# Kernel tuning notes

Measured on AMD Instinct MI355X. Metric: run time of the kernel, lower is better.

The kernel has to match this reference:

```python
import jax, jax.numpy as jnp
import numpy as np

EMB = 32
MP_ITERS = 5
N_NODES = 100000
N_EDGES = 3200000
N_FEAT = 128
N_ACT = 1024


def setup_inputs() -> dict:
    key = jax.random.key(0)
    ks = jax.random.split(key, 8)
    s = lambda fan_in: 1.0 / np.sqrt(fan_in)
    return {
        "node_feats": jax.random.normal(ks[0], (N_NODES, N_FEAT), dtype=jnp.float32),
        "edge_index": jax.random.randint(ks[1], (2, N_EDGES), 0, N_NODES, dtype=jnp.int64),
        "actionable": jax.random.randint(ks[2], (N_ACT,), 0, N_NODES, dtype=jnp.int64),
        "W_embed": jax.random.normal(ks[3], (N_FEAT, EMB), dtype=jnp.float32) * s(N_FEAT),
        "b_embed": jnp.zeros((EMB,), jnp.float32),
        "W_msg": jax.random.normal(ks[4], (EMB, EMB), dtype=jnp.float32) * s(EMB),
        "b_msg": jnp.zeros((EMB,), jnp.float32),
        "W_upd": jax.random.normal(ks[5], (2 * EMB, EMB), dtype=jnp.float32) * s(2 * EMB),
        "b_upd": jnp.zeros((EMB,), jnp.float32),
        "W_val": jax.random.normal(ks[6], (EMB, 1), dtype=jnp.float32) * s(EMB),
        "b_val": jnp.zeros((1,), jnp.float32),
        "W_pol": jax.random.normal(ks[7], (EMB, 1), dtype=jnp.float32) * s(EMB),
        "b_pol": jnp.zeros((1,), jnp.float32),
    }


def reference(node_feats, edge_index, actionable, W_embed, b_embed, W_msg, b_msg,
              W_upd, b_upd, W_val, b_val, W_pol, b_pol):
    lrelu = lambda z: jax.nn.leaky_relu(z, negative_slope=0.01)  # torch LeakyReLU default
    n = node_feats.shape[0]
    src, dst = edge_index[0], edge_index[1]
    # node embedding: (N, F) -> (N, 32)
    x = lrelu(node_feats @ W_embed + b_embed)
    # 5 message-passing iterations with shared weights:
    # m_{j->i} = MLP(x_j); agg_i = sum_j m_{j->i}; x_i' = U([x_i, agg_i])
    for _ in range(MP_ITERS):
        msgs = lrelu(x[src] @ W_msg + b_msg)               # (E, 32) gather + tiny GEMM
        agg = jax.ops.segment_sum(msgs, dst, num_segments=n)  # scatter-add -> (N, 32)
        x = lrelu(jnp.concatenate([x, agg], axis=1) @ W_upd + b_upd)
    xg = x.mean(axis=0, keepdims=True)                      # (1, 32)
    value = xg @ W_val + b_val                              # (1, 1)
    logits_all = (x @ W_pol + b_pol).ravel()                # (N,)
    probs = jax.nn.softmax(logits_all[actionable])          # (A,) action distribution
    # deterministic output: [value, action probabilities]
    return jnp.concatenate([value.ravel(), probs])
```

## Files before the change

### kernel.cpp

```cpp
#include <hip/hip_runtime.h>
#include <hip/hip_fp16.h>
#include <math.h>

#define EMB 32
#define NFEAT 128
#define RANGE 256
#define NBUCK_MAX 512
#define FILL_TILE 4096
#define FIN_CAP 12288
#define PAD_SLACK (RANGE * 10)

__device__ __forceinline__ float lrelu(float z) { return z > 0.f ? z : 0.01f * z; }

__global__ __launch_bounds__(256) void k_embed(
    const float* __restrict__ nf, const float* __restrict__ Wemb,
    const float* __restrict__ bemb, const float* __restrict__ Wmsg,
    const float* __restrict__ bmsg, float* __restrict__ x,
    __half* __restrict__ m, int n)
{
    __shared__ float sW[NFEAT * EMB];
    __shared__ float sWm[EMB * EMB];
    __shared__ float srow[8][NFEAT];
    int t = threadIdx.x;
    for (int i = t; i < NFEAT * EMB; i += 256) sW[i] = Wemb[i];
    for (int i = t; i < EMB * EMB; i += 256) sWm[i] = Wmsg[i];
    __syncthreads();

    int g = t >> 5;
    int e = t & 31;
    float be = bemb[e];
    float bm = bmsg[e];

    int per_pass = gridDim.x * 8;
    int iters = (n + per_pass - 1) / per_pass;
    for (int it = 0; it < iters; ++it) {
        int node = (it * gridDim.x + blockIdx.x) * 8 + g;
        __syncthreads();
        if (node < n) {
            float4 v = ((const float4*)(nf + (size_t)node * NFEAT))[e];
            ((float4*)&srow[g][0])[e] = v;
        }
        __syncthreads();
        if (node < n) {
            float acc = be;
            #pragma unroll
            for (int k = 0; k < NFEAT; ++k)
                acc = fmaf(srow[g][k], sW[k * EMB + e], acc);
            float xv = lrelu(acc);
            x[(size_t)node * EMB + e] = xv;
            float macc = bm;
            #pragma unroll
            for (int k = 0; k < EMB; ++k)
                macc = fmaf(__shfl(xv, k, 32), sWm[k * EMB + e], macc);
            m[(size_t)node * EMB + e] = __float2half(lrelu(macc));
        }
    }
}

__global__ __launch_bounds__(256) void k_bhist(
    const int* __restrict__ dst, int* __restrict__ bucket_cnt, int E, int nbuck)
{
    __shared__ int h[NBUCK_MAX];
    int t = threadIdx.x;
    for (int i = t; i < nbuck; i += 256) h[i] = 0;
    __syncthreads();
    for (int i = blockIdx.x * 256 + t; i < E; i += gridDim.x * 256)
        atomicAdd(&h[dst[i] >> 8], 1);
    __syncthreads();
    for (int i = t; i < nbuck; i += 256)
        if (h[i]) atomicAdd(&bucket_cnt[i], h[i]);
}

__global__ __launch_bounds__(512) void k_bscan(
    const int* __restrict__ bucket_cnt, int* __restrict__ bucket_base,
    int* __restrict__ bucket_cur, int nbuck)
{
    __shared__ int s[NBUCK_MAX];
    int t = threadIdx.x;
    int c = (t < nbuck) ? ((bucket_cnt[t] + PAD_SLACK + 16 + 15) & ~15) : 0;
    s[t] = c;
    __syncthreads();
    for (int off = 1; off < NBUCK_MAX; off <<= 1) {
        int add = (t >= off) ? s[t - off] : 0;
        __syncthreads();
        s[t] += add;
        __syncthreads();
    }
    if (t < nbuck) {
        int base = s[t] - c;
        bucket_base[t] = base;
        bucket_cur[t] = base;
    }
}

__global__ __launch_bounds__(256) void k_bfill(
    const int* __restrict__ src, const int* __restrict__ dst,
    int* __restrict__ bucket_cur, unsigned int* __restrict__ csrp, int E)
{
    __shared__ int scnt[NBUCK_MAX];
    __shared__ int gbase[NBUCK_MAX];
    int t = threadIdx.x;
    for (int i = t; i < NBUCK_MAX; i += 256) scnt[i] = 0;
    __syncthreads();

    unsigned int vals[16];
    int br[16];
    int base = blockIdx.x * FILL_TILE;
    #pragma unroll
    for (int k = 0; k < 16; ++k) {
        int e = base + k * 256 + t;
        if (e < E) {
            int d = dst[e];
            int s = src[e];
            int b = d >> 8;
            int r = atomicAdd(&scnt[b], 1);
            vals[k] = ((unsigned int)s << 8) | (unsigned int)(d & 255);
            br[k] = (b << 13) | r;
        } else br[k] = -1;
    }
    __syncthreads();
    for (int i = t; i < NBUCK_MAX; i += 256) {
        int c = scnt[i];
        gbase[i] = c ? atomicAdd(&bucket_cur[i], c) : 0;
    }
    __syncthreads();
    #pragma unroll
    for (int k = 0; k < 16; ++k) {
        if (br[k] >= 0) {
            int b = br[k] >> 13;
            int r = br[k] & 8191;
            csrp[gbase[b] + r] = vals[k];
        }
    }
}

__global__ __launch_bounds__(256) void k_csrfin(
    unsigned int* __restrict__ csrp, const int* __restrict__ bucket_base,
    const int* __restrict__ bucket_cnt, int* __restrict__ pdeg01,
    int* __restrict__ row, int n, int half)
{
    __shared__ int lh[2 * RANGE];
    __shared__ int pst[2 * RANGE];
    __shared__ int lc[2 * RANGE];
    __shared__ int psum[RANGE];
    __shared__ int ssrc[FIN_CAP];
    int bk = blockIdx.x;
    int t = threadIdx.x;
    int base = bucket_base[bk];
    int cnt = bucket_cnt[bk];
    if (cnt > FIN_CAP - PAD_SLACK) cnt = FIN_CAP - PAD_SLACK;

    lh[t] = 0;
    lh[t + RANGE] = 0;
    __syncthreads();
    for (int i = t; i < cnt; i += 256) {
        unsigned int v = csrp[base + i];
        int dl = (int)(v & 255u);
        int s = (int)(v >> 8);
        atomicAdd(&lh[dl * 2 + (s >= half ? 1 : 0)], 1);
    }
    __syncthreads();
    int c0 = lh[2 * t];
    int c1 = lh[2 * t + 1];
    int p0 = (c0 + 7) & ~7;
    int p1 = (c1 + 3) & ~3;
    psum[t] = p0 + p1;
    __syncthreads();
    for (int off = 1; off < RANGE; off <<= 1) {
        int add = (t >= off) ? psum[t - off] : 0;
        __syncthreads();
        psum[t] += add;
        __syncthreads();
    }
    int excl = psum[t] - (p0 + p1);
    pst[2 * t] = excl;
    pst[2 * t + 1] = excl + p0;
    lc[2 * t] = excl;
    lc[2 * t + 1] = excl + p0;
    int node = bk * RANGE + t;
    if (node < n) {
        row[node] = base + excl;
        pdeg01[node] = p0 | (p1 << 16);
    }
    __syncthreads();
    for (int i = t; i < cnt; i += 256) {
        unsigned int v = csrp[base + i];
        int dl = (int)(v & 255u);
        int s = (int)(v >> 8);
        int key = dl * 2 + (s >= half ? 1 : 0);
        int p = atomicAdd(&lc[key], 1);
        ssrc[p] = s;
    }
    __syncthreads();
    for (int i = c0; i < p0; ++i) ssrc[pst[2 * t] + i] = n;
    for (int i = c1; i < p1; ++i) ssrc[pst[2 * t + 1] + i] = n;
    __syncthreads();
    int ptot = psum[RANGE - 1];
    for (int i = t; i < ptot; i += 256)
        csrp[base + i] = (unsigned int)ssrc[i];
}

template<int PHASE>
__global__ __launch_bounds__(256) void k_gather(
    const __half* __restrict__ m_in, float* __restrict__ agg,
    const int* __restrict__ row, const int* __restrict__ pdeg01,
    const unsigned int* __restrict__ csrp, int n)
{
    int t = threadIdx.x;
    unsigned cp = (unsigned)(t & 15);
    int g = t >> 4;
    int groups = gridDim.x * 16;
    for (int node = blockIdx.x * 16 + g; node < n; node += groups) {
        int pd = pdeg01[node];
        int p0 = pd & 0xffff;
        float2 acc;
        if (PHASE == 0) {
            const uint4* ip = (const uint4*)(csrp + row[node]);
            int nch = p0 >> 3;
            acc.x = 0.f; acc.y = 0.f;
            for (int c = 0; c < nch; ++c) {
                uint4 ia = ip[2 * c];
                uint4 ib = ip[2 * c + 1];
                float2 f0 = __half22float2(*(const __half2*)(m_in + ia.x * 32u + 2u * cp));
                float2 f1 = __half22float2(*(const __half2*)(m_in + ia.y * 32u + 2u * cp));
                float2 f2 = __half22float2(*(const __half2*)(m_in + ia.z * 32u + 2u * cp));
                float2 f3 = __half22float2(*(const __half2*)(m_in + ia.w * 32u + 2u * cp));
                float2 f4 = __half22float2(*(const __half2*)(m_in + ib.x * 32u + 2u * cp));
                float2 f5 = __half22float2(*(const __half2*)(m_in + ib.y * 32u + 2u * cp));
                float2 f6 = __half22float2(*(const __half2*)(m_in + ib.z * 32u + 2u * cp));
                float2 f7 = __half22float2(*(const __half2*)(m_in + ib.w * 32u + 2u * cp));
                acc.x += ((f0.x + f1.x) + (f2.x + f3.x)) + ((f4.x + f5.x) + (f6.x + f7.x));
                acc.y += ((f0.y + f1.y) + (f2.y + f3.y)) + ((f4.y + f5.y) + (f6.y + f7.y));
            }
        } else {
            const uint4* ip = (const uint4*)(csrp + row[node] + p0);
            int nch = pd >> 18;
            acc = ((const float2*)agg)[(unsigned)node * 16u + cp];
            for (int c = 0; c < nch; ++c) {
                uint4 ia = ip[c];
                float2 f0 = __half22float2(*(const __half2*)(m_in + ia.x * 32u + 2u * cp));
                float2 f1 = __half22float2(*(const __half2*)(m_in + ia.y * 32u + 2u * cp));
                float2 f2 = __half22float2(*(const __half2*)(m_in + ia.z * 32u + 2u * cp));
                float2 f3 = __half22float2(*(const __half2*)(m_in + ia.w * 32u + 2u * cp));
                acc.x += (f0.x + f1.x) + (f2.x + f3.x);
                acc.y += (f0.y + f1.y) + (f2.y + f3.y);
            }
        }
        ((float2*)agg)[(unsigned)node * 16u + cp] = acc;
    }
}

__device__ __forceinline__ float2 gemm16(float2 v, const float* __restrict__ W, int cp)
{
    float2 u; u.x = 0.f; u.y = 0.f;
    #pragma unroll
    for (int kk = 0; kk < 16; ++kk) {
        float xa = __shfl(v.x, kk, 16);
        float xb = __shfl(v.y, kk, 16);
        float2 w0 = *(const float2*)&W[(2 * kk) * EMB + 2 * cp];
        float2 w1 = *(const float2*)&W[(2 * kk + 1) * EMB + 2 * cp];
        u.x = fmaf(xa, w0.x, u.x); u.y = fmaf(xa, w0.y, u.y);
        u.x = fmaf(xb, w1.x, u.x); u.y = fmaf(xb, w1.y, u.y);
    }
    return u;
}

template<int DO_MSG, int DO_COLSUM>
__global__ __launch_bounds__(256) void k_upd(
    float* __restrict__ x, const float* __restrict__ agg,
    __half* __restrict__ m_out,
    const float* __restrict__ Wupd, const float* __restrict__ bupd,
    const float* __restrict__ Wmsg, const float* __restrict__ bmsg,
    float* __restrict__ sums, int n)
{
    __shared__ float sW[2 * EMB * EMB];
    __shared__ float sWm[EMB * EMB];
    __shared__ float2 red[16][16];
    int t = threadIdx.x;
    for (int i = t; i < 2 * EMB * EMB; i += 256) sW[i] = Wupd[i];
    if (DO_MSG)
        for (int i = t; i < EMB * EMB; i += 256) sWm[i] = Wmsg[i];
    __syncthreads();

    int cp = t & 15;
    int g = t >> 4;
    float2 bu = ((const float2*)bupd)[cp];
    float2 bm2;
    if (DO_MSG) bm2 = ((const float2*)bmsg)[cp];
    float2 colacc; colacc.x = 0.f; colacc.y = 0.f;
    int groups = gridDim.x * 16;
    for (int node = blockIdx.x * 16 + g; node < n; node += groups) {
        float2 x2 = ((const float2*)x)[(unsigned)node * 16u + cp];
        float2 a2 = ((const float2*)agg)[(unsigned)node * 16u + cp];
        float2 u = gemm16(x2, sW, cp);
        float2 v = gemm16(a2, sW + EMB * EMB, cp);
        float2 xn;
        xn.x = lrelu(u.x + v.x + bu.x);
        xn.y = lrelu(u.y + v.y + bu.y);
        ((float2*)x)[(unsigned)node * 16u + cp] = xn;
        if (DO_MSG) {
            float2 mm = gemm16(xn, sWm, cp);
            mm.x = lrelu(mm.x + bm2.x);
            mm.y = lrelu(mm.y + bm2.y);
            *(__half2*)(m_out + (unsigned)node * 32u + 2u * cp) = __float22half2_rn(mm);
        }
        if (DO_COLSUM) { colacc.x += xn.x; colacc.y += xn.y; }
    }
    if (DO_COLSUM) {
        red[g][cp] = colacc;
        __syncthreads();
        if (t < 16) {
            float2 s2; s2.x = 0.f; s2.y = 0.f;
            #pragma unroll
            for (int gg = 0; gg < 16; ++gg) {
                s2.x += red[gg][t].x;
                s2.y += red[gg][t].y;
            }
            atomicAdd(&sums[2 * t], s2.x);
            atomicAdd(&sums[2 * t + 1], s2.y);
        }
    }
}

__global__ __launch_bounds__(1024) void k_head(
    const float* __restrict__ x, const int* __restrict__ act,
    const float* __restrict__ Wval, const float* __restrict__ bval,
    const float* __restrict__ Wpol, const float* __restrict__ bpol,
    const float* __restrict__ sums, float* __restrict__ out, int n, int A)
{
    __shared__ float sred[64];
    int t = threadIdx.x;
    int w = t >> 6;
    int lane = t & 63;
    int nwaves = (blockDim.x + 63) >> 6;

    float logit = -INFINITY;
    if (t < A) {
        int node = act[t];
        float acc = bpol[0];
        #pragma unroll
        for (int k = 0; k < EMB; ++k)
            acc = fmaf(x[(size_t)node * EMB + k], Wpol[k], acc);
        logit = acc;
    }
    float wm = logit;
    for (int off = 32; off; off >>= 1) wm = fmaxf(wm, __shfl_xor(wm, off, 64));
    if (lane == 0) sred[w] = wm;
    __syncthreads();
    if (t == 0) {
        float mm = -INFINITY;
        for (int i = 0; i < nwaves; ++i) mm = fmaxf(mm, sred[i]);
        sred[32] = mm;
    }
    __syncthreads();
    float bmax = sred[32];
    float ex = (t < A) ? __expf(logit - bmax) : 0.f;
    float ws = ex;
    for (int off = 32; off; off >>= 1) ws += __shfl_xor(ws, off, 64);
    if (lane == 0) sred[w] = ws;
    __syncthreads();
    if (t == 0) {
        float ss = 0.f;
        for (int i = 0; i < nwaves; ++i) ss += sred[i];
        sred[33] = ss;
        float val = bval[0];
        float inv_n = 1.f / (float)n;
        #pragma unroll
        for (int k = 0; k < EMB; ++k) val = fmaf(sums[k] * inv_n, Wval[k], val);
        out[0] = val;
    }
    __syncthreads();
    float tot = sred[33];
    if (t < A) out[1 + t] = ex / tot;
}

extern "C" void kernel_launch(void* const* d_in, const int* in_sizes, int n_in,
                              void* d_out, int out_size, void* d_ws, size_t ws_size,
                              hipStream_t stream)
{
    const float* nf   = (const float*)d_in[0];
    const int*   ei   = (const int*)d_in[1];
    const int*   act  = (const int*)d_in[2];
    const float* Wemb = (const float*)d_in[3];
    const float* bemb = (const float*)d_in[4];
    const float* Wmsg = (const float*)d_in[5];
    const float* bmsg = (const float*)d_in[6];
    const float* Wupd = (const float*)d_in[7];
    const float* bupd = (const float*)d_in[8];
    const float* Wval = (const float*)d_in[9];
    const float* bval = (const float*)d_in[10];
    const float* Wpol = (const float*)d_in[11];
    const float* bpol = (const float*)d_in[12];

    int n = in_sizes[0] / NFEAT;
    int E = in_sizes[1] / 2;
    int A = in_sizes[2];
    const int* src = ei;
    const int* dst = ei + E;
    int nbuck = (n + RANGE - 1) / RANGE;
    int half = n / 2;

    char* w = (char*)d_ws;
    auto alloc = [&](size_t bytes) -> void* {
        void* p = (void*)w;
        w += (bytes + 255) & ~(size_t)255;
        return p;
    };
    float*  x    = (float*)alloc((size_t)n * EMB * 4);
    float*  agg  = (float*)alloc((size_t)n * EMB * 4);
    __half* mA   = (__half*)alloc((size_t)(n + 1) * EMB * 2);
    __half* mB   = (__half*)alloc((size_t)(n + 1) * EMB * 2);
    int*    pdeg01 = (int*)alloc((size_t)n * 4);
    int*    row  = (int*)alloc((size_t)n * 4);
    int*    bucket_cnt  = (int*)alloc((size_t)nbuck * 4);
    int*    bucket_base = (int*)alloc((size_t)nbuck * 4);
    int*    bucket_cur  = (int*)alloc((size_t)nbuck * 4);
    unsigned int* csrp  = (unsigned int*)alloc(((size_t)E + (size_t)nbuck * (PAD_SLACK + 32)) * 4);
    float*  sums = (float*)alloc(EMB * 4);

    hipMemsetAsync(bucket_cnt, 0, (size_t)nbuck * 4, stream);
    hipMemsetAsync(sums, 0, EMB * 4, stream);
    hipMemsetAsync(mA + (size_t)n * EMB, 0, EMB * 2, stream);
    hipMemsetAsync(mB + (size_t)n * EMB, 0, EMB * 2, stream);

    const int NB = 2048;

    k_embed<<<NB, 256, 0, stream>>>(nf, Wemb, bemb, Wmsg, bmsg, x, mA, n);

    k_bhist<<<256, 256, 0, stream>>>(dst, bucket_cnt, E, nbuck);
    k_bscan<<<1, NBUCK_MAX, 0, stream>>>(bucket_cnt, bucket_base, bucket_cur, nbuck);
    int nfill = (E + FILL_TILE - 1) / FILL_TILE;
    k_bfill<<<nfill, 256, 0, stream>>>(src, dst, bucket_cur, csrp, E);
    k_csrfin<<<nbuck, 256, 0, stream>>>(csrp, bucket_base, bucket_cnt, pdeg01, row, n, half);

    __half* mi = mA;
    __half* mo = mB;
    for (int it = 0; it < 5; ++it) {
        k_gather<0><<<NB, 256, 0, stream>>>(mi, agg, row, pdeg01, csrp, n);
        k_gather<1><<<NB, 256, 0, stream>>>(mi, agg, row, pdeg01, csrp, n);
        if (it < 4)
            k_upd<1, 0><<<NB, 256, 0, stream>>>(x, agg, mo, Wupd, bupd, Wmsg, bmsg, sums, n);
        else
            k_upd<0, 1><<<NB, 256, 0, stream>>>(x, agg, mo, Wupd, bupd, Wmsg, bmsg, sums, n);
        __half* tmp = mi; mi = mo; mo = tmp;
    }

    k_head<<<1, 1024, 0, stream>>>(x, act, Wval, bval, Wpol, bpol, sums,
                                   (float*)d_out, n, A);
}
```

Baseline: 682.0 us.

## Widen per-thread vectors to 8-byte half loads in gather and embed kernels

```diff
diff --git a/kernel.cpp b/kernel.cpp
--- a/kernel.cpp
+++ b/kernel.cpp
@@ -8,7 +8,7 @@
 #define NBUCK_MAX 512
 #define FILL_TILE 4096
 #define FIN_CAP 12288
-#define PAD_SLACK (RANGE * 10)
+#define PAD_SLACK (RANGE * 14)
 
 __device__ __forceinline__ float lrelu(float z) { return z > 0.f ? z : 0.01f * z; }
 
@@ -20,40 +20,60 @@
 {
     __shared__ float sW[NFEAT * EMB];
     __shared__ float sWm[EMB * EMB];
-    __shared__ float srow[8][NFEAT];
     int t = threadIdx.x;
     for (int i = t; i < NFEAT * EMB; i += 256) sW[i] = Wemb[i];
     for (int i = t; i < EMB * EMB; i += 256) sWm[i] = Wmsg[i];
     __syncthreads();
 
-    int g = t >> 5;
-    int e = t & 31;
-    float be = bemb[e];
-    float bm = bmsg[e];
-
-    int per_pass = gridDim.x * 8;
-    int iters = (n + per_pass - 1) / per_pass;
-    for (int it = 0; it < iters; ++it) {
-        int node = (it * gridDim.x + blockIdx.x) * 8 + g;
-        __syncthreads();
-        if (node < n) {
-            float4 v = ((const float4*)(nf + (size_t)node * NFEAT))[e];
-            ((float4*)&srow[g][0])[e] = v;
-        }
-        __syncthreads();
-        if (node < n) {
-            float acc = be;
-            #pragma unroll
-            for (int k = 0; k < NFEAT; ++k)
-                acc = fmaf(srow[g][k], sW[k * EMB + e], acc);
-            float xv = lrelu(acc);
-            x[(size_t)node * EMB + e] = xv;
-            float macc = bm;
-            #pragma unroll
-            for (int k = 0; k < EMB; ++k)
-                macc = fmaf(__shfl(xv, k, 32), sWm[k * EMB + e], macc);
-            m[(size_t)node * EMB + e] = __float2half(lrelu(macc));
-        }
+    int c = t & 7;
+    int g = t >> 3;
+    float4 be = ((const float4*)bemb)[c];
+    float4 bm = ((const float4*)bmsg)[c];
+
+    int per_pass = gridDim.x * 32;
+    for (int node = blockIdx.x * 32 + g; node < n; node += per_pass) {
+        float v[16];
+        const float4* rp = (const float4*)(nf + (size_t)node * NFEAT + c * 16);
+        #pragma unroll
+        for (int q = 0; q < 4; ++q) {
+            float4 r4 = rp[q];
+            v[4 * q + 0] = r4.x; v[4 * q + 1] = r4.y;
+            v[4 * q + 2] = r4.z; v[4 * q + 3] = r4.w;
+        }
+        float4 acc = be;
+        #pragma unroll
+        for (int k = 0; k < NFEAT; ++k) {
+            float xa = __shfl(v[k & 15], k >> 4, 8);
+            float4 wv = *(const float4*)&sW[k * EMB + 4 * c];
+            acc.x = fmaf(xa, wv.x, acc.x);
+            acc.y = fmaf(xa, wv.y, acc.y);
+            acc.z = fmaf(xa, wv.z, acc.z);
+            acc.w = fmaf(xa, wv.w, acc.w);
+        }
+        float xn[4];
+        xn[0] = lrelu(acc.x); xn[1] = lrelu(acc.y);
+        xn[2] = lrelu(acc.z); xn[3] = lrelu(acc.w);
+        float4 xs; xs.x = xn[0]; xs.y = xn[1]; xs.z = xn[2]; xs.w = xn[3];
+        ((float4*)x)[(unsigned)node * 8u + (unsigned)c] = xs;
+
+        float4 ma = bm;
+        #pragma unroll
+        for (int k = 0; k < EMB; ++k) {
+            float xa = __shfl(xn[k & 3], k >> 2, 8);
+            float4 wv = *(const float4*)&sWm[k * EMB + 4 * c];
+            ma.x = fmaf(xa, wv.x, ma.x);
+            ma.y = fmaf(xa, wv.y, ma.y);
+            ma.z = fmaf(xa, wv.z, ma.z);
+            ma.w = fmaf(xa, wv.w, ma.w);
+        }
+        float2 m0; m0.x = lrelu(ma.x); m0.y = lrelu(ma.y);
+        float2 m1; m1.x = lrelu(ma.z); m1.y = lrelu(ma.w);
+        __half2 h0 = __float22half2_rn(m0);
+        __half2 h1 = __float22half2_rn(m1);
+        uint2 st;
+        st.x = *(unsigned*)&h0;
+        st.y = *(unsigned*)&h1;
+        *(uint2*)(m + (unsigned)node * 32u + 4u * (unsigned)c) = st;
     }
 }
 
@@ -163,7 +183,7 @@
     int c0 = lh[2 * t];
     int c1 = lh[2 * t + 1];
     int p0 = (c0 + 7) & ~7;
-    int p1 = (c1 + 3) & ~3;
+    int p1 = (c1 + 7) & ~7;
     psum[t] = p0 + p1;
     __syncthreads();
     for (int off = 1; off < RANGE; off <<= 1) {
@@ -200,6 +220,17 @@
         csrp[base + i] = (unsigned int)ssrc[i];
 }
 
+__device__ __forceinline__ void gacc(const __half* __restrict__ mp,
+                                     unsigned idx, unsigned c4, float4& acc)
+{
+    uint2 r = *(const uint2*)(mp + idx * 32u + c4);
+    __half2 h0 = *(__half2*)&r.x;
+    __half2 h1 = *(__half2*)&r.y;
+    float2 f0 = __half22float2(h0);
+    float2 f1 = __half22float2(h1);
+    acc.x += f0.x; acc.y += f0.y; acc.z += f1.x; acc.w += f1.y;
+}
+
 template<int PHASE>
 __global__ __launch_bounds__(256) void k_gather(
     const __half* __restrict__ m_in, float* __restrict__ agg,
@@ -207,46 +238,37 @@
     const unsigned int* __restrict__ csrp, int n)
 {
     int t = threadIdx.x;
-    unsigned cp = (unsigned)(t & 15);
-    int g = t >> 4;
-    int groups = gridDim.x * 16;
-    for (int node = blockIdx.x * 16 + g; node < n; node += groups) {
+    unsigned c4 = (unsigned)((t & 7) * 4);
+    int g = t >> 3;
+    int groups = gridDim.x * 32;
+    for (int node = blockIdx.x * 32 + g; node < n; node += groups) {
         int pd = pdeg01[node];
         int p0 = pd & 0xffff;
-        float2 acc;
+        const uint4* ip;
+        int nch;
+        float4 acc;
         if (PHASE == 0) {
-            const uint4* ip = (const uint4*)(csrp + row[node]);
-            int nch = p0 >> 3;
-            acc.x = 0.f; acc.y = 0.f;
-            for (int c = 0; c < nch; ++c) {
-                uint4 ia = ip[2 * c];
-                uint4 ib = ip[2 * c + 1];
-                float2 f0 = __half22float2(*(const __half2*)(m_in + ia.x * 32u + 2u * cp));
-                float2 f1 = __half22float2(*(const __half2*)(m_in + ia.y * 32u + 2u * cp));
-                float2 f2 = __half22float2(*(const __half2*)(m_in + ia.z * 32u + 2u * cp));
-                float2 f3 = __half22float2(*(const __half2*)(m_in + ia.w * 32u + 2u * cp));
-                float2 f4 = __half22float2(*(const __half2*)(m_in + ib.x * 32u + 2u * cp));
-                float2 f5 = __half22float2(*(const __half2*)(m_in + ib.y * 32u + 2u * cp));
-                float2 f6 = __half22float2(*(const __half2*)(m_in + ib.z * 32u + 2u * cp));
-                float2 f7 = __half22float2(*(const __half2*)(m_in + ib.w * 32u + 2u * cp));
-                acc.x += ((f0.x + f1.x) + (f2.x + f3.x)) + ((f4.x + f5.x) + (f6.x + f7.x));
-                acc.y += ((f0.y + f1.y) + (f2.y + f3.y)) + ((f4.y + f5.y) + (f6.y + f7.y));
-            }
+            ip = (const uint4*)(csrp + row[node]);
+            nch = p0 >> 3;
+            acc.x = 0.f; acc.y = 0.f; acc.z = 0.f; acc.w = 0.f;
         } else {
-            const uint4* ip = (const uint4*)(csrp + row[node] + p0);
-            int nch = pd >> 18;
-            acc = ((const float2*)agg)[(unsigned)node * 16u + cp];
-            for (int c = 0; c < nch; ++c) {
-                uint4 ia = ip[c];
-                float2 f0 = __half22float2(*(const __half2*)(m_in + ia.x * 32u + 2u * cp));
-                float2 f1 = __half22float2(*(const __half2*)(m_in + ia.y * 32u + 2u * cp));
-                float2 f2 = __half22float2(*(const __half2*)(m_in + ia.z * 32u + 2u * cp));
-                float2 f3 = __half22float2(*(const __half2*)(m_in + ia.w * 32u + 2u * cp));
-                acc.x += (f0.x + f1.x) + (f2.x + f3.x);
-                acc.y += (f0.y + f1.y) + (f2.y + f3.y);
-            }
-        }
-        ((float2*)agg)[(unsigned)node * 16u + cp] = acc;
+            ip = (const uint4*)(csrp + row[node] + p0);
+            nch = pd >> 19;
+            acc = ((const float4*)agg)[(unsigned)node * 8u + (unsigned)(t & 7)];
+        }
+        for (int cc = 0; cc < nch; ++cc) {
+            uint4 ia = ip[2 * cc];
+            uint4 ib = ip[2 * cc + 1];
+            gacc(m_in, ia.x, c4, acc);
+            gacc(m_in, ia.y, c4, acc);
+            gacc(m_in, ia.z, c4, acc);
+            gacc(m_in, ia.w, c4, acc);
+            gacc(m_in, ib.x, c4, acc);
+            gacc(m_in, ib.y, c4, acc);
+            gacc(m_in, ib.z, c4, acc);
+            gacc(m_in, ib.w, c4, acc);
+        }
+        ((float4*)agg)[(unsigned)node * 8u + (unsigned)(t & 7)] = acc;
     }
 }
 
```

Result: slower. 756.7 us (+10.9%).
